# Optimization experiments

Hardware: AMD Instinct MI355X
Metric: run time of the kernel (lower is better)

The kernel has to match this reference:

```python
import jax, jax.numpy as jnp
import numpy as np

B, L, D_MODEL, N_HEADS = 8, 256, 2048, 8
D_HEAD = D_MODEL // N_HEADS  # 256 == L, required by DeltaRuleOperator broadcasting
ALPHA0, BETA0 = 0.1, 0.9      # delta_rule_strength, 1 - strength
LN_EPS = 1e-5


def setup_inputs() -> dict:
    k = jax.random.key(0)
    ks = jax.random.split(k, 8)
    s = 0.02
    return {
        "query": jax.random.normal(ks[0], (B, L, D_MODEL), jnp.float32),
        "key": jax.random.normal(ks[1], (B, L, D_MODEL), jnp.float32),
        "value": jax.random.normal(ks[2], (B, L, D_MODEL), jnp.float32),
        "Wq": jax.random.normal(ks[3], (D_MODEL, D_MODEL), jnp.float32) * s,
        "Wk": jax.random.normal(ks[4], (D_MODEL, D_MODEL), jnp.float32) * s,
        "Wv": jax.random.normal(ks[5], (D_MODEL, D_MODEL), jnp.float32) * s,
        "Wo": jax.random.normal(ks[6], (D_MODEL, D_MODEL), jnp.float32) * s,
        "bo": jnp.zeros((D_MODEL,), jnp.float32),
        "ln_g": jnp.ones((D_MODEL,), jnp.float32),
        "ln_b": jnp.zeros((D_MODEL,), jnp.float32),
        "alpha": jnp.asarray(ALPHA0, jnp.float32),
        "beta": jnp.asarray(BETA0, jnp.float32),
    }


def reference(query, key, value, Wq, Wk, Wv, Wo, bo, ln_g, ln_b, alpha, beta):
    Bs, Ls, D = query.shape
    H, Dh = N_HEADS, D // N_HEADS

    def proj(x, W):  # torch Linear: x @ W.T, split heads -> [B,H,L,Dh]
        return (x @ W.T).reshape(Bs, Ls, H, Dh).transpose(0, 2, 1, 3)

    Q = proj(query, Wq)
    K = proj(key, Wk)
    V = proj(value, Wv)

    # DeltaRuleOperator, applied sequentially per head (buffer mutates across heads)
    kv = jnp.einsum('bhld,bhmd->bhlm', K, V)  # [B,H,L,L] with L == Dh
    kv_heads = jnp.moveaxis(kv, 1, 0)          # [H,B,L,L]

    def cs_step(cs, kv_h):
        # cumulative_state = beta*cs + alpha*detach(mean(kv)); head uses pre-update cs
        new = beta * cs + alpha * jax.lax.stop_gradient(kv_h.mean(axis=(0, 1)))
        return new, cs

    _, cs_seq = jax.lax.scan(cs_step, jnp.zeros((Dh,), query.dtype), kv_heads)  # [H,Dh]
    cs_b = cs_seq[None, :, None, :]                       # [1,H,1,Dh]
    q_mod = Q * (cs_b + alpha * (kv - cs_b))              # delta-rule modulated queries

    # elu feature map
    phi = lambda x: jax.nn.elu(x) + 1.0
    pq, pk = phi(q_mod), phi(K)

    def time_major(x):  # [B,H,L,Dh] -> [L, B*H, Dh]
        return x.reshape(Bs * H, Ls, Dh).transpose(1, 0, 2)

    pq_t, pk_t, v_t = time_major(pq), time_major(pk), time_major(V)

    def step(carry, xs):
        S, Z = carry                        # S:[N,Dh,Dh], Z:[N,Dh]
        q_i, k_i, v_i = xs                  # each [N,Dh]
        S = S + k_i[:, :, None] * v_i[:, None, :]
        Z = Z + k_i
        num = jnp.einsum('nf,nfd->nd', q_i, S)
        den = jnp.maximum(jnp.sum(q_i * Z, axis=-1), 1e-8)
        return (S, Z), num / den[:, None]

    N = Bs * H
    S0 = jnp.zeros((N, Dh, Dh), query.dtype)
    Z0 = jnp.zeros((N, Dh), query.dtype)
    _, outs = jax.lax.scan(step, (S0, Z0), (pq_t, pk_t, v_t))  # [L,N,Dh]

    attn = outs.transpose(1, 0, 2).reshape(Bs, H, Ls, Dh)
    attn = attn.transpose(0, 2, 1, 3).reshape(Bs, Ls, D)       # concat heads

    o = attn @ Wo.T + bo                  # out_proj (dropout is identity in eval)
    x = query + o                          # residual + LayerNorm
    mu = x.mean(-1, keepdims=True)
    var = jnp.mean((x - mu) ** 2, axis=-1, keepdims=True)
    return (x - mu) / jnp.sqrt(var + LN_EPS) * ln_g + ln_b
```

## Files before the change

kernel.cpp:

```cpp
#include <hip/hip_runtime.h>
#include <hip/hip_bf16.h>

using u16 = unsigned short;

typedef __bf16 bf16x8 __attribute__((ext_vector_type(8)));
typedef float  f32x4  __attribute__((ext_vector_type(4)));

typedef __attribute__((address_space(1))) void gas_void;
typedef __attribute__((address_space(3))) void las_void;

__device__ __forceinline__ float b2f(u16 u) {
  union { unsigned u; float f; } v; v.u = ((unsigned)u) << 16; return v.f;
}
__device__ __forceinline__ u16 f2b(float f) {
  union { float f; unsigned u; } v; v.f = f;
  unsigned r = v.u + 0x7fffu + ((v.u >> 16) & 1u);
  return (u16)(r >> 16);
}

__device__ __forceinline__ void gld_lds16(const u16* g, u16* l) {
  __builtin_amdgcn_global_load_lds((gas_void*)g, (las_void*)l, 16, 0, 0);
}

template <int EPI, int BK>
__global__ __launch_bounds__(256) void gemm_bt(
    const u16* __restrict__ A, int lda, long sA1, long sA2,
    const u16* __restrict__ B, int ldb, long sB1, long sB2,
    void* __restrict__ Cv, int ldc, long sC1, long sC2,
    int K, int HDIV,
    const float* __restrict__ bias, const float* __restrict__ resid,
    float* __restrict__ partOut) {
  __shared__ __align__(16) u16 lds[2 * 128 * BK];
  __shared__ float denS[128];
  const int t = threadIdx.x;
  const int lane = t & 63;
  const int wave = t >> 6;
  const int wm = wave >> 1, wn = wave & 1;
  const int laneM = lane & 15, quad = lane >> 4;
  const int zb = blockIdx.z / HDIV, zh = blockIdx.z % HDIV;

  int bx = blockIdx.x, by = blockIdx.y;
  if (EPI == 2) { by = (bx >= 1) ? 1 : 0; bx = (bx == 2) ? 1 : 0; }
  const int kEnd = (EPI == 3) ? ((by + 1) * 128 < K ? (by + 1) * 128 : K) : K;

  const u16* Abase = A + zb * sA1 + zh * sA2 + (long)by * 128 * lda;
  const u16* Bbase = B + zb * sB1 + zh * sB2 + (long)bx * 128 * ldb;

  constexpr int STEPS = BK / 16;
  constexpr int RPS = 2048 / BK;
  constexpr int KK = BK / 32;
  const int sRow = (BK == 64) ? (t >> 3) : (t >> 2);
  const int sg = (BK == 64) ? (t & 7) : (t & 3);
  const int swz = (BK == 64) ? (sg ^ (sRow & 7)) : (sg ^ ((sRow >> 1) & 3));
  const int sc = swz * 8;

  f32x4 acc[4][4];
#pragma unroll
  for (int i = 0; i < 4; ++i)
#pragma unroll
    for (int j = 0; j < 4; ++j) acc[i][j] = (f32x4){0.f, 0.f, 0.f, 0.f};
  float dsum[4] = {0.f, 0.f, 0.f, 0.f};

  for (int k0 = 0; k0 < kEnd; k0 += BK) {
#pragma unroll
    for (int p = 0; p < STEPS; ++p)
      gld_lds16(Abase + (long)(p * RPS + sRow) * lda + k0 + sc,
                &lds[p * 2048 + t * 8]);
#pragma unroll
    for (int p = 0; p < STEPS; ++p)
      gld_lds16(Bbase + (long)(p * RPS + sRow) * ldb + k0 + sc,
                &lds[128 * BK + p * 2048 + t * 8]);
    __syncthreads();
    bf16x8 af[KK][4], bfv[KK][4];
#pragma unroll
    for (int kk = 0; kk < KK; ++kk) {
      int perm8;
      if (BK == 64) perm8 = ((kk * 4 + quad) ^ (laneM & 7)) * 8;
      else          perm8 = (quad ^ ((laneM >> 1) & 3)) * 8;
#pragma unroll
      for (int i = 0; i < 4; ++i) {
        af[kk][i] = *(const bf16x8*)&lds[(wm * 64 + i * 16 + laneM) * BK + perm8];
        bfv[kk][i] =
            *(const bf16x8*)&lds[128 * BK + (wn * 64 + i * 16 + laneM) * BK + perm8];
      }
    }
    if (EPI == 3) {
#pragma unroll
      for (int kk = 0; kk < KK; ++kk)
#pragma unroll
        for (int i = 0; i < 4; ++i) {
          union { bf16x8 v; u16 s[8]; } u; u.v = af[kk][i];
          float ds = 0.f;
#pragma unroll
          for (int e = 0; e < 8; ++e) ds += b2f(u.s[e]);
          dsum[i] += ds;
        }
    }
#pragma unroll
    for (int kk = 0; kk < KK; ++kk)
#pragma unroll
      for (int i = 0; i < 4; ++i)
#pragma unroll
        for (int j = 0; j < 4; ++j)
          acc[i][j] = __builtin_amdgcn_mfma_f32_16x16x32_bf16(
              af[kk][i], bfv[kk][j], acc[i][j], 0, 0, 0);
    __syncthreads();
  }

  if (EPI == 3) {
#pragma unroll
    for (int i = 0; i < 4; ++i) {
      float s = dsum[i];
      s += __shfl_xor(s, 16);
      s += __shfl_xor(s, 32);
      if (wn == 0 && quad == 0)
        denS[wm * 64 + i * 16 + laneM] = fmaxf(s, 1e-8f);
    }
    __syncthreads();
  }

  if (EPI == 1) {
#pragma unroll
    for (int j = 0; j < 4; ++j) {
      float s = 0.f;
#pragma unroll
      for (int i = 0; i < 4; ++i)
#pragma unroll
        for (int r = 0; r < 4; ++r) s += acc[i][j][r];
      s += __shfl_xor(s, 16);
      s += __shfl_xor(s, 32);
      if (quad == 0)
        atomicAdd(&partOut[zh * 256 + bx * 128 + wn * 64 + j * 16 + laneM], s);
    }
  }

  const long cOff = zb * sC1 + zh * sC2;
  const int colB = bx * 128 + wn * 64;
#pragma unroll
  for (int i = 0; i < 4; ++i) {
#pragma unroll
    for (int j = 0; j < 4; ++j) {
#pragma unroll
      for (int r = 0; r < 4; ++r) {
        const int lrow = wm * 64 + i * 16 + quad * 4 + r;
        const int row = by * 128 + lrow;
        const int col = colB + j * 16 + laneM;
        const long idx = cOff + (long)row * ldc + col;
        float v = acc[i][j][r];
        if (EPI == 0 || EPI == 1) {
          ((u16*)Cv)[idx] = f2b(v);
        } else if (EPI == 2) {
          ((u16*)Cv)[idx] = f2b(col <= row ? v : 0.0f);
        } else if (EPI == 3) {
          ((u16*)Cv)[idx] = f2b(v / denS[lrow]);
        } else {
          ((float*)Cv)[idx] =
              (zb == 0) ? v + bias[col] + resid[(long)row * ldc + col] : v;
        }
      }
    }
  }
}

__device__ __forceinline__ void g256_tile(
    const u16* __restrict__ la, const u16* __restrict__ lb,
    u16* __restrict__ sa, u16* __restrict__ sb, int tau, int nt,
    const u16* AgR0, const u16* AgR1, const u16* BgR0, const u16* BgR1,
    int rowA, int rowB, int rg, int t, f32x4 (&acc)[8][4]) {
  const bool st = (tau + 3) < nt;
  const int ks = (tau + 3) << 5;
  bf16x8 af[4], bv[4];
#pragma unroll
  for (int m = 0; m < 4; ++m)
    af[m] = *(const bf16x8*)&la[(rowA + m * 16) * 32 + rg];
#pragma unroll
  for (int n = 0; n < 4; ++n)
    bv[n] = *(const bf16x8*)&lb[(rowB + n * 16) * 32 + rg];
  if (st) {
    gld_lds16(AgR0 + ks, &sa[t * 8]);
    gld_lds16(AgR1 + ks, &sa[4096 + t * 8]);
  }
  __builtin_amdgcn_s_barrier();
  asm volatile("s_waitcnt lgkmcnt(0)" ::: "memory");
  __builtin_amdgcn_s_setprio(1);
#pragma unroll
  for (int m = 0; m < 4; ++m)
#pragma unroll
    for (int n = 0; n < 4; ++n)
      acc[m][n] = __builtin_amdgcn_mfma_f32_16x16x32_bf16(af[m], bv[n],
                                                          acc[m][n], 0, 0, 0);
  __builtin_amdgcn_s_setprio(0);
  __builtin_amdgcn_s_barrier();
#pragma unroll
  for (int m = 0; m < 4; ++m)
    af[m] = *(const bf16x8*)&la[(rowA + 64 + m * 16) * 32 + rg];
  if (st) {
    gld_lds16(BgR0 + ks, &sb[t * 8]);
    gld_lds16(BgR1 + ks, &sb[4096 + t * 8]);
  }
  __builtin_amdgcn_s_barrier();
  asm volatile("s_waitcnt lgkmcnt(0)" ::: "memory");
  __builtin_amdgcn_s_setprio(1);
#pragma unroll
  for (int m = 0; m < 4; ++m)
#pragma unroll
    for (int n = 0; n < 4; ++n)
      acc[4 + m][n] = __builtin_amdgcn_mfma_f32_16x16x32_bf16(
          af[m], bv[n], acc[4 + m][n], 0, 0, 0);
  __builtin_amdgcn_s_setprio(0);
  if (tau < nt - 1) {
    if (tau + 3 < nt)
      asm volatile("s_waitcnt vmcnt(8)" ::: "memory");
    else if (tau + 2 < nt)
      asm volatile("s_waitcnt vmcnt(4)" ::: "memory");
    else
      asm volatile("s_waitcnt vmcnt(0)" ::: "memory");
    __builtin_amdgcn_s_barrier();
  }
}

template <int EPI>
__global__ __launch_bounds__(512) void gemm256(
    const u16* __restrict__ A, int lda, long sA1,
    const u16* __restrict__ B, int ldb, long sB1,
    void* __restrict__ Cv, int ldc, long sC1, int K,
    const float* __restrict__ bias, const float* __restrict__ resid) {
  __shared__ __align__(16) u16 A0[8192], A1[8192], A2[8192], A3[8192];
  __shared__ __align__(16) u16 B0[8192], B1[8192], B2[8192], B3[8192];
  const int t = threadIdx.x;
  const int lane = t & 63, wave = t >> 6;
  const int wm = wave >> 2, wn = wave & 3;
  const int laneM = lane & 15, quad = lane >> 4;

  const int cpx = gridDim.x >> 3;
  const int id2 = (blockIdx.x & 7) * cpx + (blockIdx.x >> 3);
  const int bx = id2 & 7, by = (id2 >> 3) & 7, z = id2 >> 6;

  const u16* Ag = A + (long)z * sA1 + (long)by * 256 * lda;
  const u16* Bg = B + (long)z * sB1 + (long)bx * 256 * ldb;

  const int nt = K >> 5;
  const int rg = (quad ^ ((laneM >> 1) & 3)) * 8;
  const int rowA = wm * 128 + laneM;
  const int rowB = wn * 64 + laneM;

  const int sRow0 = t >> 2, sRow1 = (512 + t) >> 2;
  const int sc0 = (((t) & 3) ^ ((sRow0 >> 1) & 3)) * 8;
  const int sc1 = (((512 + t) & 3) ^ ((sRow1 >> 1) & 3)) * 8;
  const u16* AgR0 = Ag + (long)sRow0 * lda + sc0;
  const u16* AgR1 = Ag + (long)sRow1 * lda + sc1;
  const u16* BgR0 = Bg + (long)sRow0 * ldb + sc0;
  const u16* BgR1 = Bg + (long)sRow1 * ldb + sc1;

  f32x4 acc[8][4];
#pragma unroll
  for (int i = 0; i < 8; ++i)
#pragma unroll
    for (int j = 0; j < 4; ++j) acc[i][j] = (f32x4){0.f, 0.f, 0.f, 0.f};

  gld_lds16(AgR0, &A0[t * 8]);      gld_lds16(AgR1, &A0[4096 + t * 8]);
  gld_lds16(BgR0, &B0[t * 8]);      gld_lds16(BgR1, &B0[4096 + t * 8]);
  gld_lds16(AgR0 + 32, &A1[t * 8]); gld_lds16(AgR1 + 32, &A1[4096 + t * 8]);
  gld_lds16(BgR0 + 32, &B1[t * 8]); gld_lds16(BgR1 + 32, &B1[4096 + t * 8]);
  gld_lds16(AgR0 + 64, &A2[t * 8]); gld_lds16(AgR1 + 64, &A2[4096 + t * 8]);
  gld_lds16(BgR0 + 64, &B2[t * 8]); gld_lds16(BgR1 + 64, &B2[4096 + t * 8]);
  asm volatile("s_waitcnt vmcnt(8)" ::: "memory");
  __builtin_amdgcn_s_barrier();

  for (int tau = 0; tau < nt; tau += 4) {
    g256_tile(A0, B0, A3, B3, tau, nt, AgR0, AgR1, BgR0, BgR1, rowA, rowB,
              rg, t, acc);
    g256_tile(A1, B1, A0, B0, tau + 1, nt, AgR0, AgR1, BgR0, BgR1, rowA,
              rowB, rg, t, acc);
    g256_tile(A2, B2, A1, B1, tau + 2, nt, AgR0, AgR1, BgR0, BgR1, rowA,
              rowB, rg, t, acc);
    g256_tile(A3, B3, A2, B2, tau + 3, nt, AgR0, AgR1, BgR0, BgR1, rowA,
              rowB, rg, t, acc);
  }

  const long cOff = (long)z * sC1;
  const int colB = bx * 256 + wn * 64;
  const int rowBase = by * 256 + wm * 128;
#pragma unroll
  for (int i = 0; i < 8; ++i) {
#pragma unroll
    for (int j = 0; j < 4; ++j) {
#pragma unroll
      for (int r = 0; r < 4; ++r) {
        const int row = rowBase + i * 16 + quad * 4 + r;
        const int col = colB + j * 16 + laneM;
        const long idx = cOff + (long)row * ldc + col;
        float v = acc[i][j][r];
        if (EPI == 0) {
          ((u16*)Cv)[idx] = f2b(v);
        } else {
          ((float*)Cv)[idx] =
              (z == 0) ? v + bias[col] + resid[(long)row * ldc + col] : v;
        }
      }
    }
  }
}

__global__ __launch_bounds__(256) void convert7(
    const float* __restrict__ s0, const float* __restrict__ s1,
    const float* __restrict__ s2, const float* __restrict__ s3,
    const float* __restrict__ s4, const float* __restrict__ s5,
    const float* __restrict__ s6, u16* __restrict__ dst) {
  long idx = (long)blockIdx.x * 256 + threadIdx.x;
  int seg = (int)(idx >> 20);
  long off = (idx & 1048575) << 2;
  const float* s;
  switch (seg) {
    case 0: s = s0; break; case 1: s = s1; break; case 2: s = s2; break;
    case 3: s = s3; break; case 4: s = s4; break; case 5: s = s5; break;
    default: s = s6;
  }
  float4 v = *(const float4*)(s + off);
  ushort4 o;
  o.x = f2b(v.x); o.y = f2b(v.y); o.z = f2b(v.z); o.w = f2b(v.w);
  *(ushort4*)(dst + (long)seg * 4194304 + off) = o;
}

__global__ __launch_bounds__(256) void pqpk_kernel(
    const u16* __restrict__ Qp, const u16* __restrict__ Kp,
    const u16* __restrict__ kv, const float* __restrict__ part,
    const float* __restrict__ alphaP, const float* __restrict__ betaP,
    u16* __restrict__ pq, u16* __restrict__ pk) {
  long base = ((long)blockIdx.x * 256 + threadIdx.x) * 8;
  int d0 = (int)(base & 255), l = (int)((base >> 8) & 255),
      h = (int)((base >> 16) & 7), b = (int)(base >> 19);
  (void)l; (void)b;
  float alpha = *alphaP, beta = *betaP;
  float cf[8] = {0.f, 0.f, 0.f, 0.f, 0.f, 0.f, 0.f, 0.f};
  for (int hh = 0; hh < h; ++hh) {
    float4 p0 = *(const float4*)(part + hh * 256 + d0);
    float4 p1 = *(const float4*)(part + hh * 256 + d0 + 4);
    const float sc = alpha * (1.0f / 2048.0f);
    cf[0] = beta * cf[0] + sc * p0.x;
    cf[1] = beta * cf[1] + sc * p0.y;
    cf[2] = beta * cf[2] + sc * p0.z;
    cf[3] = beta * cf[3] + sc * p0.w;
    cf[4] = beta * cf[4] + sc * p1.x;
    cf[5] = beta * cf[5] + sc * p1.y;
    cf[6] = beta * cf[6] + sc * p1.z;
    cf[7] = beta * cf[7] + sc * p1.w;
  }
  long pidx = base;
  pidx = ((long)((int)(base >> 19) * 256 + (int)((base >> 8) & 255))) * 2048 +
         (int)((base >> 16) & 7) * 256 + d0;
  ushort4 q0 = *(const ushort4*)(Qp + pidx);
  ushort4 q1 = *(const ushort4*)(Qp + pidx + 4);
  ushort4 k0 = *(const ushort4*)(Kp + pidx);
  ushort4 k1 = *(const ushort4*)(Kp + pidx + 4);
  ushort4 v0 = *(const ushort4*)(kv + base);
  ushort4 v1 = *(const ushort4*)(kv + base + 4);
  u16 qs[8] = {q0.x, q0.y, q0.z, q0.w, q1.x, q1.y, q1.z, q1.w};
  u16 ks[8] = {k0.x, k0.y, k0.z, k0.w, k1.x, k1.y, k1.z, k1.w};
  u16 vs[8] = {v0.x, v0.y, v0.z, v0.w, v1.x, v1.y, v1.z, v1.w};
  u16 oq[8], ok[8];
#pragma unroll
  for (int e = 0; e < 8; ++e) {
    float qm = b2f(qs[e]) * (cf[e] + alpha * (b2f(vs[e]) - cf[e]));
    oq[e] = f2b(qm > 0.f ? qm + 1.f : expf(qm));
    float Kv = b2f(ks[e]);
    ok[e] = f2b(Kv > 0.f ? Kv + 1.f : expf(Kv));
  }
  *(ushort4*)(pq + base) = (ushort4){oq[0], oq[1], oq[2], oq[3]};
  *(ushort4*)(pq + base + 4) = (ushort4){oq[4], oq[5], oq[6], oq[7]};
  *(ushort4*)(pk + base) = (ushort4){ok[0], ok[1], ok[2], ok[3]};
  *(ushort4*)(pk + base + 4) = (ushort4){ok[4], ok[5], ok[6], ok[7]};
}

__global__ __launch_bounds__(256) void vtrans_kernel(const u16* __restrict__ Vp,
                                                     u16* __restrict__ Vt) {
  __shared__ u16 tile[32][33];
  int z = blockIdx.z, b = z >> 3, h = z & 7;
  int jT = blockIdx.x * 32, dT = blockIdx.y * 32;
  int tx = threadIdx.x, ty = threadIdx.y;
#pragma unroll
  for (int ii = 0; ii < 4; ++ii) {
    int j = jT + ty + ii * 8, d = dT + tx;
    tile[ty + ii * 8][tx] = Vp[(long)(b * 256 + j) * 2048 + h * 256 + d];
  }
  __syncthreads();
#pragma unroll
  for (int ii = 0; ii < 4; ++ii) {
    int d = dT + ty + ii * 8, j = jT + tx;
    Vt[(long)z * 65536 + d * 256 + j] = tile[tx][ty + ii * 8];
  }
}

__global__ __launch_bounds__(256) void ln_kernel(
    const float* __restrict__ x0, const float* __restrict__ x1,
    const float* __restrict__ g, const float* __restrict__ bb,
    float* __restrict__ out) {
  int row = blockIdx.x, t = threadIdx.x;
  const float4* xr0 = (const float4*)(x0 + (long)row * 2048);
  const float4* xr1 = (const float4*)(x1 + (long)row * 2048);
  float4 a0 = xr0[t], b0 = xr1[t], a1 = xr0[t + 256], b1 = xr1[t + 256];
  float4 v0, v1;
  v0.x = a0.x + b0.x; v0.y = a0.y + b0.y; v0.z = a0.z + b0.z; v0.w = a0.w + b0.w;
  v1.x = a1.x + b1.x; v1.y = a1.y + b1.y; v1.z = a1.z + b1.z; v1.w = a1.w + b1.w;
  float s = v0.x + v0.y + v0.z + v0.w + v1.x + v1.y + v1.z + v1.w;
  float ss = v0.x * v0.x + v0.y * v0.y + v0.z * v0.z + v0.w * v0.w +
             v1.x * v1.x + v1.y * v1.y + v1.z * v1.z + v1.w * v1.w;
  for (int o = 32; o; o >>= 1) { s += __shfl_xor(s, o); ss += __shfl_xor(ss, o); }
  __shared__ float a1s[4], a2s[4];
  int wave = t >> 6, lane = t & 63;
  if (lane == 0) { a1s[wave] = s; a2s[wave] = ss; }
  __syncthreads();
  s = a1s[0] + a1s[1] + a1s[2] + a1s[3];
  ss = a2s[0] + a2s[1] + a2s[2] + a2s[3];
  float mu = s * (1.f / 2048.f);
  float var = ss * (1.f / 2048.f) - mu * mu;
  float rstd = rsqrtf(var + 1e-5f);
  const float4* g4 = (const float4*)g;
  const float4* b4 = (const float4*)bb;
  float4* orow = (float4*)(out + (long)row * 2048);
  float4 gg = g4[t], bv = b4[t], r;
  r.x = (v0.x - mu) * rstd * gg.x + bv.x;
  r.y = (v0.y - mu) * rstd * gg.y + bv.y;
  r.z = (v0.z - mu) * rstd * gg.z + bv.z;
  r.w = (v0.w - mu) * rstd * gg.w + bv.w;
  orow[t] = r;
  gg = g4[t + 256]; bv = b4[t + 256];
  r.x = (v1.x - mu) * rstd * gg.x + bv.x;
  r.y = (v1.y - mu) * rstd * gg.y + bv.y;
  r.z = (v1.z - mu) * rstd * gg.z + bv.z;
  r.w = (v1.w - mu) * rstd * gg.w + bv.w;
  orow[t + 256] = r;
}

extern "C" void kernel_launch(void* const* d_in, const int* in_sizes, int n_in,
                              void* d_out, int out_size, void* d_ws,
                              size_t ws_size, hipStream_t stream) {
  const float* query = (const float*)d_in[0];
  const float* key = (const float*)d_in[1];
  const float* value = (const float*)d_in[2];
  const float* Wq = (const float*)d_in[3];
  const float* Wk = (const float*)d_in[4];
  const float* Wv = (const float*)d_in[5];
  const float* Wo = (const float*)d_in[6];
  const float* bo = (const float*)d_in[7];
  const float* ln_g = (const float*)d_in[8];
  const float* ln_b = (const float*)d_in[9];
  const float* alphaP = (const float*)d_in[10];
  const float* betaP = (const float*)d_in[11];

  char* ws = (char*)d_ws;
  const long SZ = 8388608;
  u16* qb = (u16*)(ws);
  u16* Wb = (u16*)(ws + 3 * SZ);
  u16* Qp = (u16*)(ws + 7 * SZ);
  u16* kvb = (u16*)(ws + 10 * SZ);
  u16* pq = (u16*)(ws + 12 * SZ);
  u16* pk = (u16*)(ws + 13 * SZ);
  u16* Vt = (u16*)(ws + 14 * SZ);
  u16* attnb = (u16*)(ws + 15 * SZ);
  u16* Ab = (u16*)(ws + 10 * SZ);
  float* x0 = (float*)(ws + 12 * SZ);
  float* x1 = (float*)(ws);
  float* part = (float*)(ws + 16 * SZ);

  u16* Kp = Qp + 4194304;
  u16* Vp = Qp + 8388608;
  u16* Wob = Wb + 3 * 4194304;

  hipMemsetAsync(part, 0, 8 * 256 * sizeof(float), stream);

  convert7<<<28672, 256, 0, stream>>>(query, key, value, Wq, Wk, Wv, Wo, qb);

  gemm256<0><<<dim3(192, 1, 1), 512, 0, stream>>>(
      qb, 2048, 4194304L, Wb, 2048, 4194304L, (void*)Qp, 2048, 4194304L,
      2048, nullptr, nullptr);

  gemm_bt<1, 64><<<dim3(2, 2, 64), 256, 0, stream>>>(
      Kp, 2048, 524288L, 256L, Vp, 2048, 524288L, 256L, (void*)kvb, 256,
      524288L, 65536L, 256, 8, nullptr, nullptr, part);

  pqpk_kernel<<<2048, 256, 0, stream>>>(Qp, Kp, kvb, part, alphaP, betaP,
                                        pq, pk);

  gemm_bt<2, 64><<<dim3(3, 1, 64), 256, 0, stream>>>(
      pq, 256, 524288L, 65536L, pk, 256, 524288L, 65536L, (void*)Ab, 256,
      524288L, 65536L, 256, 8, nullptr, nullptr, nullptr);

  vtrans_kernel<<<dim3(8, 8, 64), dim3(32, 8), 0, stream>>>(Vp, Vt);

  gemm_bt<3, 64><<<dim3(2, 2, 64), 256, 0, stream>>>(
      Ab, 256, 524288L, 65536L, Vt, 256, 524288L, 65536L, (void*)attnb, 2048,
      524288L, 256L, 256, 8, nullptr, nullptr, nullptr);

  gemm256<4><<<dim3(128, 1, 1), 512, 0, stream>>>(
      attnb, 2048, 1024L, Wob, 2048, 1024L, (void*)x0, 2048, -25165824L,
      1024, bo, query);

  ln_kernel<<<2048, 256, 0, stream>>>(x0, x1, ln_g, ln_b, (float*)d_out);
}
```

Measured before the change: 340.1 us.

## Fuse causal score and AV GEMMs into one flash-style linear attention kernel

Replaces the two-GEMM path (pq·pkᵀ into a materialized bf16 score matrix, then score·V with denominator) with one kernel. Per 64-row query tile it computes masked scores chunk by chunk in LDS, accumulates row sums for the denominator, and multiplies by double-buffered V tiles. This removes the score-matrix round trip through global memory and one launch. The cost is a grid of only 256 blocks with uneven causal work (nj = by+1), which may underuse the GPU.

After: 334.1 us. Within noise of the previous version (-1.8%).

```diff
diff --git a/kernel.cpp b/kernel.cpp
--- a/kernel.cpp
+++ b/kernel.cpp
@@ -302,6 +302,145 @@
   }
 }
 
+__global__ __launch_bounds__(512) void fused_av(
+    const u16* __restrict__ pq, const u16* __restrict__ pk,
+    const u16* __restrict__ Vt, u16* __restrict__ attnb) {
+  __shared__ __align__(16) u16 PQ[64 * 256];
+  __shared__ __align__(16) u16 PK[64 * 256];
+  __shared__ __align__(16) u16 VT0[256 * 64];
+  __shared__ __align__(16) u16 VT1[256 * 64];
+  __shared__ __align__(16) u16 SL[64 * 72];
+  __shared__ float denS[64];
+  const int t = threadIdx.x;
+  const int lane = t & 63, wave = t >> 6;
+  const int wm = wave >> 2, wn = wave & 3;
+  const int laneM = lane & 15, quad = lane >> 4;
+  const int by = blockIdx.x, z = blockIdx.z;
+  const int nj = by + 1;
+  const long zo = (long)z * 65536;
+
+  const u16* pqg = pq + zo + (long)by * 64 * 256;
+  const u16* pkg = pk + zo;
+  const u16* vtg = Vt + zo;
+
+#pragma unroll
+  for (int p = 0; p < 4; ++p) {
+    int c = p * 512 + t, r = c >> 5, g = c & 31;
+    gld_lds16(pqg + r * 256 + ((g ^ (r & 7)) * 8), &PQ[c * 8]);
+  }
+#pragma unroll
+  for (int p = 0; p < 4; ++p) {
+    int c = p * 512 + t, r = c >> 5, g = c & 31;
+    gld_lds16(pkg + r * 256 + ((g ^ (r & 7)) * 8), &PK[c * 8]);
+  }
+#pragma unroll
+  for (int p = 0; p < 4; ++p) {
+    int c = p * 512 + t, r = c >> 3, g = c & 7;
+    gld_lds16(vtg + r * 256 + ((g ^ (r & 7)) * 8), &VT0[c * 8]);
+  }
+  asm volatile("s_waitcnt vmcnt(0)" ::: "memory");
+  __builtin_amdgcn_s_barrier();
+
+  f32x4 acc[2][4];
+#pragma unroll
+  for (int i = 0; i < 2; ++i)
+#pragma unroll
+    for (int j = 0; j < 4; ++j) acc[i][j] = (f32x4){0.f, 0.f, 0.f, 0.f};
+  float dsum[2] = {0.f, 0.f};
+
+  for (int jt = 0; jt < nj; ++jt) {
+    const u16* VT = (jt & 1) ? VT1 : VT0;
+    u16* VTn = (jt & 1) ? VT0 : VT1;
+    f32x4 s0 = (f32x4){0.f, 0.f, 0.f, 0.f};
+    f32x4 s1 = (f32x4){0.f, 0.f, 0.f, 0.f};
+#pragma unroll
+    for (int kk = 0; kk < 8; ++kk) {
+      const int pg = ((kk * 4 + quad) ^ (laneM & 7)) * 8;
+      bf16x8 bk = *(const bf16x8*)&PK[(wn * 16 + laneM) * 256 + pg];
+      bf16x8 a0 = *(const bf16x8*)&PQ[(wm * 32 + laneM) * 256 + pg];
+      bf16x8 a1 = *(const bf16x8*)&PQ[(wm * 32 + 16 + laneM) * 256 + pg];
+      s0 = __builtin_amdgcn_mfma_f32_16x16x32_bf16(a0, bk, s0, 0, 0, 0);
+      s1 = __builtin_amdgcn_mfma_f32_16x16x32_bf16(a1, bk, s1, 0, 0, 0);
+    }
+    {
+      const int jcol = jt * 64 + wn * 16 + laneM;
+#pragma unroll
+      for (int r = 0; r < 4; ++r) {
+        int l0 = wm * 32 + quad * 4 + r;
+        int l1 = l0 + 16;
+        SL[l0 * 72 + wn * 16 + laneM] =
+            f2b(jcol <= by * 64 + l0 ? s0[r] : 0.f);
+        SL[l1 * 72 + wn * 16 + laneM] =
+            f2b(jcol <= by * 64 + l1 ? s1[r] : 0.f);
+      }
+    }
+    __builtin_amdgcn_s_barrier();
+    const bool st = (jt + 1) < nj;
+    if (st) {
+#pragma unroll
+      for (int p = 0; p < 4; ++p) {
+        int c = p * 512 + t, r = c >> 5, g = c & 31;
+        gld_lds16(pkg + ((jt + 1) * 64 + r) * 256 + ((g ^ (r & 7)) * 8),
+                  &PK[c * 8]);
+      }
+#pragma unroll
+      for (int p = 0; p < 4; ++p) {
+        int c = p * 512 + t, r = c >> 3, g = c & 7;
+        gld_lds16(vtg + r * 256 + (jt + 1) * 64 + ((g ^ (r & 7)) * 8),
+                  &VTn[c * 8]);
+      }
+    }
+#pragma unroll
+    for (int kk = 0; kk < 2; ++kk) {
+#pragma unroll
+      for (int i = 0; i < 2; ++i) {
+        bf16x8 sa = *(const bf16x8*)&SL[(wm * 32 + i * 16 + laneM) * 72 +
+                                        kk * 32 + quad * 8];
+        union { bf16x8 v; u16 s[8]; } u; u.v = sa;
+        float ds = 0.f;
+#pragma unroll
+        for (int e = 0; e < 8; ++e) ds += b2f(u.s[e]);
+        dsum[i] += ds;
+#pragma unroll
+        for (int jj = 0; jj < 4; ++jj) {
+          const int drow = wn * 64 + jj * 16 + laneM;
+          bf16x8 vb = *(const bf16x8*)&VT[drow * 64 +
+                                          (((kk * 4 + quad) ^ (laneM & 7)) * 8)];
+          acc[i][jj] =
+              __builtin_amdgcn_mfma_f32_16x16x32_bf16(sa, vb, acc[i][jj], 0, 0, 0);
+        }
+      }
+    }
+    if (st) asm volatile("s_waitcnt vmcnt(0)" ::: "memory");
+    __builtin_amdgcn_s_barrier();
+  }
+
+#pragma unroll
+  for (int i = 0; i < 2; ++i) {
+    float s = dsum[i];
+    s += __shfl_xor(s, 16);
+    s += __shfl_xor(s, 32);
+    if (wn == 0 && quad == 0)
+      denS[wm * 32 + i * 16 + laneM] = fmaxf(s, 1e-8f);
+  }
+  __builtin_amdgcn_s_barrier();
+
+  const long obase =
+      ((long)(z >> 3) * 256 + by * 64) * 2048 + (z & 7) * 256;
+#pragma unroll
+  for (int i = 0; i < 2; ++i) {
+#pragma unroll
+    for (int jj = 0; jj < 4; ++jj) {
+#pragma unroll
+      for (int r = 0; r < 4; ++r) {
+        const int lrow = wm * 32 + i * 16 + quad * 4 + r;
+        const int d = wn * 64 + jj * 16 + laneM;
+        attnb[obase + (long)lrow * 2048 + d] = f2b(acc[i][jj][r] / denS[lrow]);
+      }
+    }
+  }
+}
+
 __global__ __launch_bounds__(256) void convert7(
     const float* __restrict__ s0, const float* __restrict__ s1,
     const float* __restrict__ s2, const float* __restrict__ s3,
@@ -328,9 +467,7 @@
     const float* __restrict__ alphaP, const float* __restrict__ betaP,
     u16* __restrict__ pq, u16* __restrict__ pk) {
   long base = ((long)blockIdx.x * 256 + threadIdx.x) * 8;
-  int d0 = (int)(base & 255), l = (int)((base >> 8) & 255),
-      h = (int)((base >> 16) & 7), b = (int)(base >> 19);
-  (void)l; (void)b;
+  int d0 = (int)(base & 255), h = (int)((base >> 16) & 7);
   float alpha = *alphaP, beta = *betaP;
   float cf[8] = {0.f, 0.f, 0.f, 0.f, 0.f, 0.f, 0.f, 0.f};
   for (int hh = 0; hh < h; ++hh) {
@@ -346,9 +483,8 @@
     cf[6] = beta * cf[6] + sc * p1.z;
     cf[7] = beta * cf[7] + sc * p1.w;
   }
-  long pidx = base;
-  pidx = ((long)((int)(base >> 19) * 256 + (int)((base >> 8) & 255))) * 2048 +
-         (int)((base >> 16) & 7) * 256 + d0;
+  long pidx = ((long)((int)(base >> 19) * 256 + (int)((base >> 8) & 255))) * 2048 +
+              h * 256 + d0;
   ushort4 q0 = *(const ushort4*)(Qp + pidx);
   ushort4 q1 = *(const ushort4*)(Qp + pidx + 4);
   ushort4 k0 = *(const ushort4*)(Kp + pidx);
@@ -458,7 +594,6 @@
   u16* pk = (u16*)(ws + 13 * SZ);
   u16* Vt = (u16*)(ws + 14 * SZ);
   u16* attnb = (u16*)(ws + 15 * SZ);
-  u16* Ab = (u16*)(ws + 10 * SZ);
   float* x0 = (float*)(ws + 12 * SZ);
   float* x1 = (float*)(ws);
   float* part = (float*)(ws + 16 * SZ);
@@ -482,15 +617,9 @@
   pqpk_kernel<<<2048, 256, 0, stream>>>(Qp, Kp, kvb, part, alphaP, betaP,
                                         pq, pk);
 
-  gemm_bt<2, 64><<<dim3(3, 1, 64), 256, 0, stream>>>(
-      pq, 256, 524288L, 65536L, pk, 256, 524288L, 65536L, (void*)Ab, 256,
-      524288L, 65536L, 256, 8, nullptr, nullptr, nullptr);
-
   vtrans_kernel<<<dim3(8, 8, 64), dim3(32, 8), 0, stream>>>(Vp, Vt);
 
-  gemm_bt<3, 64><<<dim3(2, 2, 64), 256, 0, stream>>>(
-      Ab, 256, 524288L, 65536L, Vt, 256, 524288L, 65536L, (void*)attnb, 2048,
-      524288L, 256L, 256, 8, nullptr, nullptr, nullptr);
+  fused_av<<<dim3(4, 1, 64), 512, 0, stream>>>(pq, pk, Vt, attnb);
 
   gemm256<4><<<dim3(128, 1, 1), 512, 0, stream>>>(
       attnb, 2048, 1024L, Wob, 2048, 1024L, (void*)x0, 2048, -25165824L,
```
